# Kernel tuning notes

Measured on AMD Instinct MI355X. Metric: run time of the kernel, lower is better.

The kernel has to match this reference:

```python
import jax, jax.numpy as jnp
import numpy as np

N = 50000      # nodes
E = 1200000    # edges (before self loops)
IN = 128       # in_channels
HID = 32       # hidden_channels
HEADS = 2
HC = HID * HEADS  # 64, per-layer output channels
OUT = 40       # classes
NEG_SLOPE = 0.2
BN_EPS = 1e-5


def setup_inputs() -> dict:
    key = jax.random.key(0)
    ks = jax.random.split(key, 20)
    def nrm(k, shape, scale=0.1):
        return jax.random.normal(k, shape, dtype=jnp.float32) * scale
    return {
        "x": jax.random.normal(ks[0], (N, IN), dtype=jnp.float32),
        "edge_index": jax.random.randint(ks[1], (2, E), 0, N),
        "W1": nrm(ks[2], (IN, HC)),
        "a_src1": nrm(ks[3], (HEADS, HID)),
        "a_dst1": nrm(ks[4], (HEADS, HID)),
        "b1": nrm(ks[5], (HC,)),
        "bn_gamma": 1.0 + nrm(ks[6], (HC,)),
        "bn_beta": nrm(ks[7], (HC,)),
        "bn_mean": nrm(ks[8], (HC,)),
        "bn_var": jax.random.uniform(ks[9], (HC,), minval=0.5, maxval=1.5),
        "W2": nrm(ks[10], (HC, HC)),
        "a_src2": nrm(ks[11], (HEADS, HID)),
        "a_dst2": nrm(ks[12], (HEADS, HID)),
        "b2": nrm(ks[13], (HC,)),
        "Wf": nrm(ks[14], (HC, OUT)),
        "bf": nrm(ks[15], (OUT,)),
    }


def _gat_conv(x, src, dst, W, a_s, a_d, b):
    # x: [N, F_in] -> h: [N, H, C]
    h = (x @ W).reshape(N, HEADS, HID)
    alpha_src = jnp.einsum("nhc,hc->nh", h, a_s)  # [N, H]
    alpha_dst = jnp.einsum("nhc,hc->nh", h, a_d)  # [N, H]
    e = alpha_src[src] + alpha_dst[dst]            # [E, H]
    e = jnp.where(e > 0, e, NEG_SLOPE * e)         # leaky_relu(0.2)
    # scatter softmax over edges grouped by dst node
    m = jax.ops.segment_max(e, dst, num_segments=N)
    m = jnp.where(jnp.isfinite(m), m, 0.0)         # isolated nodes -> -inf fill
    ee = jnp.exp(e - m[dst])
    denom = jax.ops.segment_sum(ee, dst, num_segments=N)
    alpha = ee / (denom[dst] + 1e-16)              # [E, H]
    # gather src features, weight by attention, scatter-add to dst
    out = jax.ops.segment_sum(h[src] * alpha[:, :, None], dst, num_segments=N)
    return out.reshape(N, HC) + b                  # concat heads + bias


def reference(x, edge_index, W1, a_src1, a_dst1, b1, bn_gamma, bn_beta,
              bn_mean, bn_var, W2, a_src2, a_dst2, b2, Wf, bf):
    # PyG GATConv adds self loops by default
    loop = jnp.arange(N, dtype=edge_index.dtype)
    src = jnp.concatenate([edge_index[0], loop])
    dst = jnp.concatenate([edge_index[1], loop])

    x1 = _gat_conv(x, src, dst, W1, a_src1, a_dst1, b1)
    x1 = (x1 - bn_mean) / jnp.sqrt(bn_var + BN_EPS) * bn_gamma + bn_beta  # BN eval
    x1 = jax.nn.elu(x1)
    # dropout is identity in eval mode
    x2 = _gat_conv(x1, src, dst, W2, a_src2, a_dst2, b2)
    jk = jnp.maximum(x1, x2)  # JumpingKnowledge 'max'
    logits = jk @ Wf + bf
    return jax.nn.log_softmax(logits, axis=1)
```

## Files before the change

### kernel.cpp

```cpp
#include <hip/hip_runtime.h>
#include <hip/hip_bf16.h>
#include <math.h>

#define N_NODES 50000
#define E_EDGES 1200000
#define E_TOT   (E_EDGES + N_NODES)
#define NEG_SLOPE 0.2f
#define BN_EPS 1e-5f
#define P_PART 196
#define B1 64
#define NSCAN (P_PART * B1)

__device__ __forceinline__ int rl_i(int v, int l) {
    return __builtin_amdgcn_readlane(v, l);
}
__device__ __forceinline__ float rl_f(float v, int l) {
    return __uint_as_float(__builtin_amdgcn_readlane(__float_as_uint(v), l));
}
__device__ __forceinline__ unsigned bf16_bits(float f) {
    unsigned u = __float_as_uint(f);
    return (u + 0x7FFFu + ((u >> 16) & 1u)) >> 16;
}

__global__ void hist_kernel(const int* __restrict__ edst, unsigned* __restrict__ Ghist) {
    __shared__ unsigned hist[P_PART];
    for (int i = threadIdx.x; i < P_PART; i += 256) hist[i] = 0;
    __syncthreads();
    const int chunk = (E_TOT + B1 - 1) / B1;
    const int beg = blockIdx.x * chunk;
    const int end = min(beg + chunk, E_TOT);
    for (int i = beg + threadIdx.x; i < end; i += 256) {
        int d = (i < E_EDGES) ? edst[i] : (i - E_EDGES);
        atomicAdd(&hist[d >> 8], 1u);
    }
    __syncthreads();
    for (int p = threadIdx.x; p < P_PART; p += 256)
        Ghist[p * B1 + blockIdx.x] = hist[p];
}

__global__ void scan2_kernel(const unsigned* __restrict__ Ghist, unsigned* __restrict__ Goff) {
    __shared__ unsigned lds[1024];
    const int t = threadIdx.x;
    const int C = (NSCAN + 1023) / 1024;
    const int beg = t * C;
    const int end = min(beg + C, NSCAN);
    unsigned sum = 0;
    for (int i = beg; i < end; ++i) sum += Ghist[i];
    lds[t] = sum;
    __syncthreads();
    for (int off = 1; off < 1024; off <<= 1) {
        unsigned x = (t >= off) ? lds[t - off] : 0;
        __syncthreads();
        lds[t] += x;
        __syncthreads();
    }
    unsigned run = (t == 0) ? 0 : lds[t - 1];
    for (int i = beg; i < end; ++i) { Goff[i] = run; run += Ghist[i]; }
}

__global__ void partbase_kernel(const unsigned* __restrict__ Goff,
                                int* __restrict__ partbase, int* __restrict__ ptr) {
    int p = threadIdx.x;
    if (p < P_PART) partbase[p] = (int)Goff[p * B1];
    if (p == P_PART) partbase[P_PART] = E_TOT;
    if (p == 0) ptr[N_NODES] = E_TOT;
}

__global__ void scat2_kernel(const int* __restrict__ esrc, const int* __restrict__ edst,
                             const unsigned* __restrict__ Goff, unsigned* __restrict__ Gpart) {
    __shared__ unsigned cur[P_PART];
    for (int p = threadIdx.x; p < P_PART; p += 256) cur[p] = Goff[p * B1 + blockIdx.x];
    __syncthreads();
    const int chunk = (E_TOT + B1 - 1) / B1;
    const int beg = blockIdx.x * chunk;
    const int end = min(beg + chunk, E_TOT);
    for (int i = beg + threadIdx.x; i < end; i += 256) {
        int s = (i < E_EDGES) ? esrc[i] : (i - E_EDGES);
        int d = (i < E_EDGES) ? edst[i] : (i - E_EDGES);
        unsigned slot = atomicAdd(&cur[d >> 8], 1u);
        Gpart[slot] = ((unsigned)(d & 255) << 16) | (unsigned)s;
    }
}

__global__ void csr_kernel(const int* __restrict__ partbase, const unsigned* __restrict__ Gpart,
                           int* __restrict__ ptr, unsigned* __restrict__ srec) {
    __shared__ unsigned deg[256];
    __shared__ unsigned scn[256];
    const int p = blockIdx.x;
    const int t = threadIdx.x;
    const int base = partbase[p];
    const int cnt = partbase[p + 1] - base;
    deg[t] = 0;
    __syncthreads();
    for (int i = t; i < cnt; i += 256)
        atomicAdd(&deg[Gpart[base + i] >> 16], 1u);
    __syncthreads();
    unsigned v = deg[t];
    scn[t] = v;
    __syncthreads();
    for (int o = 1; o < 256; o <<= 1) {
        unsigned x = (t >= o) ? scn[t - o] : 0;
        __syncthreads();
        scn[t] += x;
        __syncthreads();
    }
    unsigned excl = scn[t] - v;
    int node = p * 256 + t;
    if (node < N_NODES) ptr[node] = base + (int)excl;
    __syncthreads();
    deg[t] = excl;
    __syncthreads();
    for (int i = t; i < cnt; i += 256) {
        unsigned rec = Gpart[base + i];
        unsigned slot = atomicAdd(&deg[rec >> 16], 1u);
        srec[base + slot] = rec;
    }
}

__global__ void ew_kernel(const int* __restrict__ partbase,
                          const unsigned* __restrict__ srec,
                          const float2* __restrict__ asrc,
                          const float2* __restrict__ adst,
                          uint2* __restrict__ wrec) {
    __shared__ float2 sad[256];
    const int p = blockIdx.x >> 2, q = blockIdx.x & 3;
    const int t = threadIdx.x;
    {
        int node = p * 256 + t;
        sad[t] = (node < N_NODES) ? adst[node] : make_float2(0.f, 0.f);
    }
    __syncthreads();
    const int base = partbase[p];
    const int cnt = partbase[p + 1] - base;
    const int qbeg = base + (cnt * q) / 4;
    const int qend = base + (cnt * (q + 1)) / 4;
    for (int i = qbeg + t; i < qend; i += 256) {
        unsigned rec = srec[i];
        int s  = (int)(rec & 0xFFFFu);
        int dl = (int)(rec >> 16);
        float2 a = asrc[s];
        float2 b = sad[dl];
        float e0 = a.x + b.x; e0 = e0 > 0.f ? e0 : NEG_SLOPE * e0;
        float e1 = a.y + b.y; e1 = e1 > 0.f ? e1 : NEG_SLOPE * e1;
        wrec[i] = make_uint2((unsigned)s,
                             bf16_bits(__expf(e0)) | (bf16_bits(__expf(e1)) << 16));
    }
}

template<int K>
__global__ __launch_bounds__(256) void lin_att_kernel(
        const float* __restrict__ x, const float* __restrict__ W,
        const float* __restrict__ a_s, const float* __restrict__ a_d,
        __hip_bfloat16* __restrict__ h, float* __restrict__ asrc,
        float* __restrict__ adst) {
    __shared__ float sx[64 * (K + 1)];
    __shared__ float sW[K * 64];
    const int tid = threadIdx.x;
    for (int i = tid; i < K * 64; i += 256) sW[i] = W[i];
    const int ng = tid >> 4;
    const int cg = tid & 15;
    const int c0 = cg * 4;
    const float4 asv = *(const float4*)&a_s[c0];
    const float4 adv = *(const float4*)&a_d[c0];
    const int ntiles = (N_NODES + 63) / 64;
    for (int tile = blockIdx.x; tile < ntiles; tile += gridDim.x) {
        const int nbase = tile * 64;
        __syncthreads();
        for (int i = tid; i < 64 * K; i += 256) {
            int n = i / K, k = i - n * K;
            int node = nbase + n;
            sx[n * (K + 1) + k] = (node < N_NODES) ? x[(size_t)node * K + k] : 0.f;
        }
        __syncthreads();
        float acc[4][4] = {};
        #pragma unroll 4
        for (int k = 0; k < K; ++k) {
            float4 wv = *(const float4*)&sW[k * 64 + c0];
            #pragma unroll
            for (int j = 0; j < 4; ++j) {
                float xv = sx[(ng * 4 + j) * (K + 1) + k];
                acc[j][0] = fmaf(xv, wv.x, acc[j][0]);
                acc[j][1] = fmaf(xv, wv.y, acc[j][1]);
                acc[j][2] = fmaf(xv, wv.z, acc[j][2]);
                acc[j][3] = fmaf(xv, wv.w, acc[j][3]);
            }
        }
        #pragma unroll
        for (int j = 0; j < 4; ++j) {
            int node = nbase + ng * 4 + j;
            float ps = acc[j][0] * asv.x + acc[j][1] * asv.y +
                       acc[j][2] * asv.z + acc[j][3] * asv.w;
            float pd = acc[j][0] * adv.x + acc[j][1] * adv.y +
                       acc[j][2] * adv.z + acc[j][3] * adv.w;
            #pragma unroll
            for (int o = 1; o < 8; o <<= 1) {
                ps += __shfl_xor(ps, o, 64);
                pd += __shfl_xor(pd, o, 64);
            }
            if (node < N_NODES) {
                ushort4 pk;
                pk.x = (unsigned short)bf16_bits(acc[j][0]);
                pk.y = (unsigned short)bf16_bits(acc[j][1]);
                pk.z = (unsigned short)bf16_bits(acc[j][2]);
                pk.w = (unsigned short)bf16_bits(acc[j][3]);
                *(ushort4*)&h[(size_t)node * 64 + c0] = pk;
                if ((cg & 7) == 0) {
                    int head = cg >> 3;
                    asrc[node * 2 + head] = ps;
                    adst[node * 2 + head] = pd;
                }
            }
        }
    }
}

template<bool BN, bool FINAL>
__global__ void gat_agg_kernel(const int* __restrict__ ptr,
                               const uint2* __restrict__ wrec,
                               const __hip_bfloat16* __restrict__ h,
                               const float* __restrict__ bias,
                               const float* __restrict__ gamma, const float* __restrict__ beta,
                               const float* __restrict__ mean, const float* __restrict__ var,
                               float* __restrict__ out,
                               const float* __restrict__ x1, const float* __restrict__ Wf,
                               const float* __restrict__ bf, float* __restrict__ out40) {
    __shared__ float sWf[FINAL ? 64 * 40 : 1];
    if constexpr (FINAL) {
        for (int i = threadIdx.x; i < 64 * 40; i += 256) sWf[i] = Wf[i];
        __syncthreads();
    }
    int node = blockIdx.x * 4 + (threadIdx.x >> 6);
    if (node >= N_NODES) return;
    const int lane = threadIdx.x & 63;
    const int half = lane & 31;
    const unsigned shl = (lane < 32) ? 16u : 0u;
    float acc = 0.f, s = 0.f;
    const int beg = ptr[node], end = ptr[node + 1];

#define EDGE(J) {                                                            \
        unsigned rx = (unsigned)rl_i((int)rec.x, (J));                       \
        unsigned ry = (unsigned)rl_i((int)rec.y, (J));                       \
        const __hip_bfloat16* hp = h + (size_t)rx * 64u;                     \
        float wv = __uint_as_float((ry << shl) & 0xFFFF0000u);               \
        acc = fmaf(wv, __bfloat162float(hp[lane]), acc);                     \
        s += wv; }

    for (int base = beg; base < end; base += 32) {
        const int cnt = min(32, end - base);
        uint2 rec = make_uint2(0u, 0u);
        if (half < cnt) rec = wrec[base + half];
        int j = 0;
        for (; j + 8 <= cnt; j += 8) {
            EDGE(j) EDGE(j + 1) EDGE(j + 2) EDGE(j + 3)
            EDGE(j + 4) EDGE(j + 5) EDGE(j + 6) EDGE(j + 7)
        }
        for (; j < cnt; ++j) { EDGE(j) }
    }
#undef EDGE

    float v = acc / (s + 1e-16f) + bias[lane];
    if constexpr (BN) {
        v = (v - mean[lane]) * rsqrtf(var[lane] + BN_EPS) * gamma[lane] + beta[lane];
        v = v > 0.f ? v : (__expf(v) - 1.f);
    }
    if constexpr (FINAL) {
        float jk = fmaxf(x1[node * 64 + lane], v);
        const int o = (lane < 40) ? lane : 0;
        float dot = 0.f;
        #pragma unroll
        for (int c = 0; c < 64; ++c) {
            float jv = rl_f(jk, c);
            dot = fmaf(jv, sWf[c * 40 + o], dot);
        }
        float logit = (lane < 40) ? (dot + bf[o]) : -INFINITY;
        float mx = logit;
        #pragma unroll
        for (int mm = 1; mm < 64; mm <<= 1) mx = fmaxf(mx, __shfl_xor(mx, mm, 64));
        float ex = (lane < 40) ? __expf(logit - mx) : 0.f;
        float sum = ex;
        #pragma unroll
        for (int mm = 1; mm < 64; mm <<= 1) sum += __shfl_xor(sum, mm, 64);
        if (lane < 40) out40[node * 40 + lane] = logit - mx - logf(sum);
    } else {
        out[node * 64 + lane] = v;
    }
}

extern "C" void kernel_launch(void* const* d_in, const int* in_sizes, int n_in,
                              void* d_out, int out_size, void* d_ws, size_t ws_size,
                              hipStream_t stream) {
    const float* x     = (const float*)d_in[0];
    const int*   ei    = (const int*)d_in[1];
    const float* W1    = (const float*)d_in[2];
    const float* as1   = (const float*)d_in[3];
    const float* ad1   = (const float*)d_in[4];
    const float* b1    = (const float*)d_in[5];
    const float* gamma = (const float*)d_in[6];
    const float* beta  = (const float*)d_in[7];
    const float* mean  = (const float*)d_in[8];
    const float* var   = (const float*)d_in[9];
    const float* W2    = (const float*)d_in[10];
    const float* as2   = (const float*)d_in[11];
    const float* ad2   = (const float*)d_in[12];
    const float* b2    = (const float*)d_in[13];
    const float* Wf    = (const float*)d_in[14];
    const float* bf    = (const float*)d_in[15];
    float* out = (float*)d_out;
    const int* esrc = ei;
    const int* edst = ei + E_EDGES;

    char* ws = (char*)d_ws;
    size_t off = 0;
    auto alloc = [&](size_t bytes) {
        char* p = ws + off;
        off += (bytes + 255) & ~(size_t)255;
        return p;
    };
    unsigned* Ghist = (unsigned*)alloc((size_t)NSCAN * 4);
    unsigned* Goff  = (unsigned*)alloc((size_t)NSCAN * 4);
    int* partbase   = (int*)alloc((size_t)(P_PART + 1) * 4);
    unsigned* Gpart = (unsigned*)alloc((size_t)E_TOT * 4);
    int* ptr              = (int*)alloc((size_t)(N_NODES + 1) * 4);
    unsigned* srec        = (unsigned*)alloc((size_t)E_TOT * 4);
    uint2* wrec           = (uint2*)alloc((size_t)E_TOT * 8);
    __hip_bfloat16* hbuf  = (__hip_bfloat16*)alloc((size_t)N_NODES * 64 * 2);
    float* x1buf = (float*)alloc((size_t)N_NODES * 64 * 4);
    float* asrc  = (float*)alloc((size_t)N_NODES * 2 * 4);
    float* adst  = (float*)alloc((size_t)N_NODES * 2 * 4);
    (void)ws_size; (void)in_sizes; (void)n_in; (void)out_size;

    const int NB = (N_NODES + 3) / 4;
    const int GT = (N_NODES + 63) / 64;

    hist_kernel<<<B1, 256, 0, stream>>>(edst, Ghist);
    scan2_kernel<<<1, 1024, 0, stream>>>(Ghist, Goff);
    partbase_kernel<<<1, 256, 0, stream>>>(Goff, partbase, ptr);
    scat2_kernel<<<B1, 256, 0, stream>>>(esrc, edst, Goff, Gpart);
    csr_kernel<<<P_PART, 256, 0, stream>>>(partbase, Gpart, ptr, srec);

    lin_att_kernel<128><<<GT, 256, 0, stream>>>(x, W1, as1, ad1, hbuf, asrc, adst);
    ew_kernel<<<P_PART * 4, 256, 0, stream>>>(partbase, srec,
        (const float2*)asrc, (const float2*)adst, wrec);
    gat_agg_kernel<true, false><<<NB, 256, 0, stream>>>(ptr, wrec, hbuf,
        b1, gamma, beta, mean, var, x1buf, nullptr, nullptr, nullptr, nullptr);

    lin_att_kernel<64><<<GT, 256, 0, stream>>>(x1buf, W2, as2, ad2, hbuf, asrc, adst);
    ew_kernel<<<P_PART * 4, 256, 0, stream>>>(partbase, srec,
        (const float2*)asrc, (const float2*)adst, wrec);
    gat_agg_kernel<false, true><<<NB, 256, 0, stream>>>(ptr, wrec, hbuf,
        b2, nullptr, nullptr, nullptr, nullptr, nullptr, x1buf, Wf, bf, out);
}
```

Before: 261.0 us.

## Process four edges per wavefront in GAT aggregation with 8-byte bf16 row loads

Restructures the aggregation kernel so each wavefront splits into four 16-lane slots. Each slot handles a different edge and each lane loads four bf16 channels (8 bytes) at a time, with a cross-slot shuffle reduction at the end. This replaces the previous scheme of one edge per wavefront iteration with readlane broadcasts and 2-byte loads, aiming to raise memory-level parallelism and cut per-edge instruction overhead. The cost is extra shuffle reductions and vectorized epilogue handling, plus a small padding of the edge-record buffer for the tail over-read.

```diff
diff --git a/kernel.cpp b/kernel.cpp
--- a/kernel.cpp
+++ b/kernel.cpp
@@ -232,45 +232,84 @@
     int node = blockIdx.x * 4 + (threadIdx.x >> 6);
     if (node >= N_NODES) return;
     const int lane = threadIdx.x & 63;
-    const int half = lane & 31;
-    const unsigned shl = (lane < 32) ? 16u : 0u;
-    float acc = 0.f, s = 0.f;
+    const int slot = lane >> 4;
+    const int cg   = lane & 15;
+    const int c0 = cg * 4;
+    const unsigned shl = (cg < 8) ? 16u : 0u;
+    const unsigned coff = (unsigned)(cg * 8);
+    const char* hb = (const char*)h;
+    float a0 = 0.f, a1 = 0.f, a2 = 0.f, a3 = 0.f, s = 0.f;
     const int beg = ptr[node], end = ptr[node + 1];
-
-#define EDGE(J) {                                                            \
-        unsigned rx = (unsigned)rl_i((int)rec.x, (J));                       \
-        unsigned ry = (unsigned)rl_i((int)rec.y, (J));                       \
-        const __hip_bfloat16* hp = h + (size_t)rx * 64u;                     \
-        float wv = __uint_as_float((ry << shl) & 0xFFFF0000u);               \
-        acc = fmaf(wv, __bfloat162float(hp[lane]), acc);                     \
+    const int deg = end - beg;
+    const uint2* rp = wrec + beg + slot;
+    const int nfull = deg >> 2;
+
+#define GRP(R) {                                                             \
+        float wv = __uint_as_float(((R).y << shl) & 0xFFFF0000u);            \
+        uint2 hh = *(const uint2*)(hb + (((R).x << 7) + coff));              \
+        a0 = fmaf(wv, __uint_as_float(hh.x << 16), a0);                      \
+        a1 = fmaf(wv, __uint_as_float(hh.x & 0xFFFF0000u), a1);              \
+        a2 = fmaf(wv, __uint_as_float(hh.y << 16), a2);                      \
+        a3 = fmaf(wv, __uint_as_float(hh.y & 0xFFFF0000u), a3);              \
         s += wv; }
 
-    for (int base = beg; base < end; base += 32) {
-        const int cnt = min(32, end - base);
-        uint2 rec = make_uint2(0u, 0u);
-        if (half < cnt) rec = wrec[base + half];
-        int j = 0;
-        for (; j + 8 <= cnt; j += 8) {
-            EDGE(j) EDGE(j + 1) EDGE(j + 2) EDGE(j + 3)
-            EDGE(j + 4) EDGE(j + 5) EDGE(j + 6) EDGE(j + 7)
-        }
-        for (; j < cnt; ++j) { EDGE(j) }
-    }
-#undef EDGE
-
-    float v = acc / (s + 1e-16f) + bias[lane];
+    int g = 0;
+    for (; g + 2 <= nfull; g += 2) {
+        uint2 r0 = rp[g * 4];
+        uint2 r1 = rp[g * 4 + 4];
+        GRP(r0) GRP(r1)
+    }
+    if (g < nfull) { uint2 r0 = rp[g * 4]; GRP(r0) }
+    const int rem = deg & 3;
+    if (rem) {
+        uint2 r0 = rp[nfull * 4];
+        if (slot >= rem) r0 = make_uint2(0u, 0u);
+        GRP(r0)
+    }
+#undef GRP
+
+    #pragma unroll
+    for (int o = 16; o < 64; o <<= 1) {
+        a0 += __shfl_xor(a0, o, 64);
+        a1 += __shfl_xor(a1, o, 64);
+        a2 += __shfl_xor(a2, o, 64);
+        a3 += __shfl_xor(a3, o, 64);
+        s  += __shfl_xor(s, o, 64);
+    }
+    const float inv = 1.f / (s + 1e-16f);
+    float4 bv = *(const float4*)&bias[c0];
+    float v0 = a0 * inv + bv.x;
+    float v1 = a1 * inv + bv.y;
+    float v2 = a2 * inv + bv.z;
+    float v3 = a3 * inv + bv.w;
     if constexpr (BN) {
-        v = (v - mean[lane]) * rsqrtf(var[lane] + BN_EPS) * gamma[lane] + beta[lane];
-        v = v > 0.f ? v : (__expf(v) - 1.f);
+        float4 mn = *(const float4*)&mean[c0];
+        float4 vr = *(const float4*)&var[c0];
+        float4 gm = *(const float4*)&gamma[c0];
+        float4 bt = *(const float4*)&beta[c0];
+        v0 = (v0 - mn.x) * rsqrtf(vr.x + BN_EPS) * gm.x + bt.x;
+        v1 = (v1 - mn.y) * rsqrtf(vr.y + BN_EPS) * gm.y + bt.y;
+        v2 = (v2 - mn.z) * rsqrtf(vr.z + BN_EPS) * gm.z + bt.z;
+        v3 = (v3 - mn.w) * rsqrtf(vr.w + BN_EPS) * gm.w + bt.w;
+        v0 = v0 > 0.f ? v0 : (__expf(v0) - 1.f);
+        v1 = v1 > 0.f ? v1 : (__expf(v1) - 1.f);
+        v2 = v2 > 0.f ? v2 : (__expf(v2) - 1.f);
+        v3 = v3 > 0.f ? v3 : (__expf(v3) - 1.f);
     }
     if constexpr (FINAL) {
-        float jk = fmaxf(x1[node * 64 + lane], v);
+        float4 x1v = *(const float4*)&x1[(size_t)node * 64 + c0];
+        float jk0 = fmaxf(x1v.x, v0);
+        float jk1 = fmaxf(x1v.y, v1);
+        float jk2 = fmaxf(x1v.z, v2);
+        float jk3 = fmaxf(x1v.w, v3);
         const int o = (lane < 40) ? lane : 0;
         float dot = 0.f;
         #pragma unroll
-        for (int c = 0; c < 64; ++c) {
-            float jv = rl_f(jk, c);
-            dot = fmaf(jv, sWf[c * 40 + o], dot);
+        for (int c = 0; c < 64; c += 4) {
+            dot = fmaf(rl_f(jk0, c >> 2), sWf[(c + 0) * 40 + o], dot);
+            dot = fmaf(rl_f(jk1, c >> 2), sWf[(c + 1) * 40 + o], dot);
+            dot = fmaf(rl_f(jk2, c >> 2), sWf[(c + 2) * 40 + o], dot);
+            dot = fmaf(rl_f(jk3, c >> 2), sWf[(c + 3) * 40 + o], dot);
         }
         float logit = (lane < 40) ? (dot + bf[o]) : -INFINITY;
         float mx = logit;
@@ -282,7 +321,10 @@
         for (int mm = 1; mm < 64; mm <<= 1) sum += __shfl_xor(sum, mm, 64);
         if (lane < 40) out40[node * 40 + lane] = logit - mx - logf(sum);
     } else {
-        out[node * 64 + lane] = v;
+        if (slot == 0) {
+            float4 v4 = make_float4(v0, v1, v2, v3);
+            *(float4*)&out[(size_t)node * 64 + c0] = v4;
+        }
     }
 }
 
@@ -322,7 +364,7 @@
     unsigned* Gpart = (unsigned*)alloc((size_t)E_TOT * 4);
     int* ptr              = (int*)alloc((size_t)(N_NODES + 1) * 4);
     unsigned* srec        = (unsigned*)alloc((size_t)E_TOT * 4);
-    uint2* wrec           = (uint2*)alloc((size_t)E_TOT * 8);
+    uint2* wrec           = (uint2*)alloc(((size_t)E_TOT + 64) * 8);
     __hip_bfloat16* hbuf  = (__hip_bfloat16*)alloc((size_t)N_NODES * 64 * 2);
     float* x1buf = (float*)alloc((size_t)N_NODES * 64 * 4);
     float* asrc  = (float*)alloc((size_t)N_NODES * 2 * 4);
```

New measurement: 259.9 us. No clear change (-0.4%).
